# Performance work log

Measured on AMD Instinct MI355X. Metric: run time of the kernel, lower is better.

The kernel has to match this reference:

```python
import jax, jax.numpy as jnp
import numpy as np

V = 32000   # vocab_size
T = 2048    # train_len (pos embed table size)
E = 1024    # embed_dim
H = 16      # num_heads
FF = 4096   # ff_dim
L = 4       # num_layers
B, C = 2, 1024
D = E // H  # head_dim = 64
EPS = 1e-5


def setup_inputs() -> dict:
    key = jax.random.key(0)
    ks = jax.random.split(key, 12)
    s = 0.02
    inp = {
        "x": jax.random.randint(ks[0], (B, C), 0, V),
        "embed": jax.random.normal(ks[1], (V, E), jnp.float32) * s,
        "pos_embed": jax.random.normal(ks[2], (T, E), jnp.float32) * s,
        "Wq": jax.random.normal(ks[3], (L, E, E), jnp.float32) * s,
        "Wk": jax.random.normal(ks[4], (L, E, E), jnp.float32) * s,
        "Wv": jax.random.normal(ks[5], (L, E, E), jnp.float32) * s,
        "Wo": jax.random.normal(ks[6], (L, E, E), jnp.float32) * s,
        "ln1_w": jnp.ones((L, E), jnp.float32),
        "ln1_b": jnp.zeros((L, E), jnp.float32),
        "ln2_w": jnp.ones((L, E), jnp.float32),
        "ln2_b": jnp.zeros((L, E), jnp.float32),
        "W1": jax.random.normal(ks[7], (L, E, FF), jnp.float32) * s,
        "b1": jnp.zeros((L, FF), jnp.float32),
        "W2": jax.random.normal(ks[8], (L, FF, E), jnp.float32) * s,
        "b2": jnp.zeros((L, E), jnp.float32),
        "lnf_w": jnp.ones((E,), jnp.float32),
        "lnf_b": jnp.zeros((E,), jnp.float32),
        "Wout": jax.random.normal(ks[9], (E, V), jnp.float32) * s,
        "bout": jnp.zeros((V,), jnp.float32),
    }
    return inp


def _layernorm(h, w, b):
    mu = jnp.mean(h, axis=-1, keepdims=True)
    var = jnp.var(h, axis=-1, keepdims=True)
    return (h - mu) * jax.lax.rsqrt(var + EPS) * w + b


def reference(x, embed, pos_embed, Wq, Wk, Wv, Wo, ln1_w, ln1_b, ln2_w, ln2_b,
              W1, b1, W2, b2, lnf_w, lnf_b, Wout, bout):
    Bx, Cx = x.shape
    positions = jnp.clip(jnp.arange(Cx), 0, T - 1)  # 'clamp' extrapolation
    h = embed[x] + pos_embed[positions]             # [B,C,E]
    # causal mask: -inf above the diagonal
    mask = jnp.where(jnp.tril(jnp.ones((Cx, Cx), bool)), 0.0, -jnp.inf).astype(h.dtype)
    scale = 1.0 / np.sqrt(D)
    for i in range(L):
        hn = _layernorm(h, ln1_w[i], ln1_b[i])
        Q = (hn @ Wq[i]).reshape(Bx, Cx, H, D).transpose(0, 2, 1, 3)  # [B,H,C,D]
        K = (hn @ Wk[i]).reshape(Bx, Cx, H, D).transpose(0, 2, 1, 3)
        Vv = (hn @ Wv[i]).reshape(Bx, Cx, H, D).transpose(0, 2, 1, 3)
        scores = jnp.einsum('bhqd,bhkd->bhqk', Q, K) * scale + mask
        weights = jax.nn.softmax(scores, axis=-1)
        attn = jnp.einsum('bhqk,bhkd->bhqd', weights, Vv)
        attn = attn.transpose(0, 2, 1, 3).reshape(Bx, Cx, E) @ Wo[i]
        h = h + attn
        hn2 = _layernorm(h, ln2_w[i], ln2_b[i])
        h = h + jax.nn.gelu(hn2 @ W1[i] + b1[i], approximate=False) @ W2[i] + b2[i]
    return _layernorm(h, lnf_w, lnf_b) @ Wout + bout  # [B,C,V]
```

## Files before the change

kernel.cpp:

```cpp
#include <hip/hip_runtime.h>
#include <hip/hip_bf16.h>
#include <math.h>

constexpr int V  = 32000;
constexpr int E  = 1024;
constexpr int H  = 16;
constexpr int FF = 4096;
constexpr int L  = 4;
constexpr int B  = 2;
constexpr int C  = 1024;
constexpr int D  = 64;
constexpr int N  = B * C;
constexpr int E3 = 3 * E;
constexpr float EPS = 1e-5f;

typedef __hip_bfloat16 bf16;
typedef __bf16 bf16x8 __attribute__((ext_vector_type(8)));
typedef __bf16 bf16x4 __attribute__((ext_vector_type(4)));
typedef float  f32x4  __attribute__((ext_vector_type(4)));

#define AS1 __attribute__((address_space(1)))
#define AS3 __attribute__((address_space(3)))

__device__ inline bf16x8 lds_load8(const bf16* p) {
    bf16x4 lo = *(const bf16x4*)p;
    bf16x4 hi = *(const bf16x4*)(p + 4);
    bf16x8 r;
    r[0]=lo[0]; r[1]=lo[1]; r[2]=lo[2]; r[3]=lo[3];
    r[4]=hi[0]; r[5]=hi[1]; r[6]=hi[2]; r[7]=hi[3];
    return r;
}
__device__ inline void lds_store8(bf16* p, bf16x8 v) {
    bf16x4 lo, hi;
    lo[0]=v[0]; lo[1]=v[1]; lo[2]=v[2]; lo[3]=v[3];
    hi[0]=v[4]; hi[1]=v[5]; hi[2]=v[6]; hi[3]=v[7];
    *(bf16x4*)p = lo; *(bf16x4*)(p + 4) = hi;
}

__device__ inline bf16x8 lds_frag32(const bf16* sbase, int row, int c) {
    return *(const bf16x8*)(sbase + row * 32 + ((c ^ ((row >> 1) & 3)) << 3));
}
__device__ inline bf16x8 lds_frag64(const bf16* sbase, int row, int c) {
    return *(const bf16x8*)(sbase + row * 64 + ((c ^ (row & 7)) << 3));
}

__global__ void embed_kernel(const int* __restrict__ x,
                             const float* __restrict__ embed,
                             const float* __restrict__ pos,
                             float* __restrict__ h) {
    int token = blockIdx.x;
    int c = token % C;
    int id = x[token];
    const float* erow = embed + (size_t)id * E;
    const float* prow = pos   + (size_t)c  * E;
    float* hrow = h + (size_t)token * E;
    for (int e = threadIdx.x; e < E; e += blockDim.x)
        hrow[e] = erow[e] + prow[e];
}

__global__ void layernorm_kernel(const float* __restrict__ in,
                                 const float* __restrict__ w,
                                 const float* __restrict__ b,
                                 bf16* __restrict__ out) {
    __shared__ float red[256];
    int token = blockIdx.x;
    int tid = threadIdx.x;
    float4 xv = ((const float4*)(in + (size_t)token * E))[tid];

    red[tid] = xv.x + xv.y + xv.z + xv.w;
    __syncthreads();
    for (int st = 128; st > 0; st >>= 1) {
        if (tid < st) red[tid] += red[tid + st];
        __syncthreads();
    }
    float mu = red[0] * (1.0f / E);
    __syncthreads();

    float d0 = xv.x - mu, d1 = xv.y - mu, d2 = xv.z - mu, d3 = xv.w - mu;
    red[tid] = d0 * d0 + d1 * d1 + d2 * d2 + d3 * d3;
    __syncthreads();
    for (int st = 128; st > 0; st >>= 1) {
        if (tid < st) red[tid] += red[tid + st];
        __syncthreads();
    }
    float var = red[0] * (1.0f / E);
    float inv = rsqrtf(var + EPS);

    float4 wv = ((const float4*)w)[tid];
    float4 bv = ((const float4*)b)[tid];
    float y0 = d0 * inv * wv.x + bv.x;
    float y1 = d1 * inv * wv.y + bv.y;
    float y2 = d2 * inv * wv.z + bv.z;
    float y3 = d3 * inv * wv.w + bv.w;
    ushort4 o;
    { bf16 t0 = __float2bfloat16(y0); o.x = *(ushort*)&t0; }
    { bf16 t1 = __float2bfloat16(y1); o.y = *(ushort*)&t1; }
    { bf16 t2 = __float2bfloat16(y2); o.z = *(ushort*)&t2; }
    { bf16 t3 = __float2bfloat16(y3); o.w = *(ushort*)&t3; }
    ((ushort4*)(out + (size_t)token * E))[tid] = o;
}

__global__ void transpose_all(const float* __restrict__ Wq,
                              const float* __restrict__ Wk,
                              const float* __restrict__ Wv,
                              const float* __restrict__ Wo,
                              const float* __restrict__ W1,
                              const float* __restrict__ W2,
                              const float* __restrict__ Wout,
                              bf16* __restrict__ qkvt, bf16* __restrict__ wot,
                              bf16* __restrict__ w1t,  bf16* __restrict__ w2t,
                              bf16* __restrict__ wvt) {
    __shared__ float tile[64][65];
    int b = blockIdx.x;
    const float* src; bf16* dst;
    int Nn, Kk, n0, k0;
    if (b >= 12288) {
        int rem = b - 12288;
        src = Wout; dst = wvt; Nn = V; Kk = E;
        n0 = (rem % 500) * 64; k0 = (rem / 500) * 64;
    } else {
        int i = b / 3072, r = b % 3072;
        if (r < 1024) {
            int mat = r >> 8, rr = r & 255;
            n0 = (rr & 15) * 64; k0 = (rr >> 4) * 64;
            Nn = E; Kk = E;
            const float* srcs[4] = {Wq, Wk, Wv, Wo};
            src = srcs[mat] + (size_t)i * E * E;
            dst = (mat < 3) ? qkvt + ((size_t)i * E3 + (size_t)mat * E) * E
                            : wot + (size_t)i * E * E;
        } else if (r < 2048) {
            int rr = r - 1024;
            n0 = (rr & 63) * 64; k0 = (rr >> 6) * 64;
            Nn = FF; Kk = E;
            src = W1 + (size_t)i * E * FF;
            dst = w1t + (size_t)i * FF * E;
        } else {
            int rr = r - 2048;
            n0 = (rr & 15) * 64; k0 = (rr >> 4) * 64;
            Nn = E; Kk = FF;
            src = W2 + (size_t)i * FF * E;
            dst = w2t + (size_t)i * E * FF;
        }
    }
    int tid = threadIdx.x;
    #pragma unroll
    for (int it = 0; it < 4; ++it) {
        int idx = it * 256 + tid;
        int row = idx >> 4, c4 = (idx & 15) * 4;
        *(float4*)&tile[row][c4] =
            *(const float4*)&src[(size_t)(k0 + row) * Nn + n0 + c4];
    }
    __syncthreads();
    #pragma unroll
    for (int it = 0; it < 2; ++it) {
        int s = it * 256 + tid;
        int nrow = s >> 3, kc = s & 7;
        bf16x8 v;
        #pragma unroll
        for (int j = 0; j < 8; ++j)
            v[j] = (__bf16)__float2bfloat16(tile[kc * 8 + j][nrow]);
        *(bf16x8*)&dst[(size_t)(n0 + nrow) * Kk + k0 + kc * 8] = v;
    }
}

__global__ void transpose_v(const bf16* __restrict__ qkv,
                            bf16* __restrict__ vt) {
    __shared__ ushort tile[32][34];
    int c0 = blockIdx.x * 32;
    int d0 = (blockIdx.y & 1) * 32;
    int bh = blockIdx.y >> 1;
    int bb = bh >> 4, hh = bh & 15;
    int tx = threadIdx.x & 31, ty = threadIdx.x >> 5;
    const ushort* src = (const ushort*)qkv;
    ushort* dst = (ushort*)vt;
    #pragma unroll
    for (int i = 0; i < 32; i += 8)
        tile[ty + i][tx] = src[(size_t)(bb * C + c0 + ty + i) * E3 + 2 * E + hh * D + d0 + tx];
    __syncthreads();
    #pragma unroll
    for (int i = 0; i < 32; i += 8)
        dst[((size_t)bh * D + d0 + ty + i) * C + c0 + tx] = tile[tx][ty + i];
}

__launch_bounds__(512, 2)
__global__ void gemm_v8(const bf16* __restrict__ A,
                        const bf16* __restrict__ Bt,
                        const float* __restrict__ bias,
                        float* __restrict__ outF,
                        int M, int Nc, int K) {
    __shared__ __align__(16) bf16 sA[2][2][128 * 64];
    __shared__ __align__(16) bf16 sB[2][2][128 * 64];

    int tid  = threadIdx.x;
    int lane = tid & 63;
    int wid  = tid >> 6;
    int wm   = wid >> 2;
    int wn   = wid & 3;
    int l16  = lane & 15;
    int lhi  = lane >> 4;

    int nwg = gridDim.x * gridDim.y;
    int id  = blockIdx.y * gridDim.x + blockIdx.x;
    int cpx = nwg >> 3;
    int swz = (id & 7) * cpx + (id >> 3);
    int bx  = swz / gridDim.y;
    int by  = swz % gridDim.y;

    size_t brow = (size_t)by * 256;
    size_t bcol = (size_t)bx * 256;

    f32x4 acc[8][4] = {};

    auto stageA = [&](int buf, int half, int t) {
        size_t k0 = (size_t)t * 64;
        #pragma unroll
        for (int j = 0; j < 2; ++j) {
            int s = j * 512 + tid;
            int row = s >> 3;
            int ch  = (s & 7) ^ (row & 7);
            int ldso = (j * 512 + wid * 64) * 8;
            const bf16* g = A + (brow + half * 128 + row) * K + k0 + ch * 8;
            __builtin_amdgcn_global_load_lds(
                (const AS1 void*)g, (AS3 void*)(&sA[buf][half][0] + ldso), 16, 0, 0);
        }
    };
    auto stageB = [&](int buf, int half, int t) {
        size_t k0 = (size_t)t * 64;
        #pragma unroll
        for (int j = 0; j < 2; ++j) {
            int s = j * 512 + tid;
            int row = s >> 3;
            int ch  = (s & 7) ^ (row & 7);
            int ldso = (j * 512 + wid * 64) * 8;
            const bf16* g = Bt + (bcol + half * 128 + row) * K + k0 + ch * 8;
            __builtin_amdgcn_global_load_lds(
                (const AS1 void*)g, (AS3 void*)(&sB[buf][half][0] + ldso), 16, 0, 0);
        }
    };

    int NT = K / 64;
    stageA(0, 0, 0); stageB(0, 0, 0); stageB(0, 1, 0); stageA(0, 1, 0);

    bf16x8 ra[4][2], rb[2][2];

    for (int t = 0; t < NT; ++t) {
        int cur = t & 1, nxt = cur ^ 1;
        int ts = (t + 1 < NT) ? t + 1 : t;

        stageA(nxt, 0, ts);
        asm volatile("s_waitcnt vmcnt(6)" ::: "memory");
        __builtin_amdgcn_sched_barrier(0);
        __builtin_amdgcn_s_barrier();
        #pragma unroll
        for (int m = 0; m < 4; ++m)
            #pragma unroll
            for (int kh = 0; kh < 2; ++kh)
                ra[m][kh] = lds_frag64(&sA[cur][0][0], wm * 64 + m * 16 + l16, kh * 4 + lhi);
        #pragma unroll
        for (int n = 0; n < 2; ++n)
            #pragma unroll
            for (int kh = 0; kh < 2; ++kh)
                rb[n][kh] = lds_frag64(&sB[cur][0][0], wn * 32 + n * 16 + l16, kh * 4 + lhi);
        __builtin_amdgcn_s_setprio(1);
        #pragma unroll
        for (int m = 0; m < 4; ++m)
            #pragma unroll
            for (int n = 0; n < 2; ++n)
                #pragma unroll
                for (int kh = 0; kh < 2; ++kh)
                    acc[m][n] = __builtin_amdgcn_mfma_f32_16x16x32_bf16(
                        ra[m][kh], rb[n][kh], acc[m][n], 0, 0, 0);
        __builtin_amdgcn_s_setprio(0);

        stageB(nxt, 0, ts);
        asm volatile("s_waitcnt vmcnt(6)" ::: "memory");
        __builtin_amdgcn_sched_barrier(0);
        __builtin_amdgcn_s_barrier();
        #pragma unroll
        for (int n = 0; n < 2; ++n)
            #pragma unroll
            for (int kh = 0; kh < 2; ++kh)
                rb[n][kh] = lds_frag64(&sB[cur][1][0], wn * 32 + n * 16 + l16, kh * 4 + lhi);
        __builtin_amdgcn_s_setprio(1);
        #pragma unroll
        for (int m = 0; m < 4; ++m)
            #pragma unroll
            for (int n = 0; n < 2; ++n)
                #pragma unroll
                for (int kh = 0; kh < 2; ++kh)
                    acc[m][n + 2] = __builtin_amdgcn_mfma_f32_16x16x32_bf16(
                        ra[m][kh], rb[n][kh], acc[m][n + 2], 0, 0, 0);
        __builtin_amdgcn_s_setprio(0);

        stageB(nxt, 1, ts);
        asm volatile("s_waitcnt vmcnt(6)" ::: "memory");
        __builtin_amdgcn_sched_barrier(0);
        __builtin_amdgcn_s_barrier();
        #pragma unroll
        for (int m = 0; m < 4; ++m)
            #pragma unroll
            for (int kh = 0; kh < 2; ++kh)
                ra[m][kh] = lds_frag64(&sA[cur][1][0], wm * 64 + m * 16 + l16, kh * 4 + lhi);
        __builtin_amdgcn_s_setprio(1);
        #pragma unroll
        for (int m = 0; m < 4; ++m)
            #pragma unroll
            for (int n = 0; n < 2; ++n)
                #pragma unroll
                for (int kh = 0; kh < 2; ++kh)
                    acc[m + 4][n + 2] = __builtin_amdgcn_mfma_f32_16x16x32_bf16(
                        ra[m][kh], rb[n][kh], acc[m + 4][n + 2], 0, 0, 0);
        __builtin_amdgcn_s_setprio(0);

        stageA(nxt, 1, ts);
        asm volatile("s_waitcnt vmcnt(6)" ::: "memory");
        __builtin_amdgcn_sched_barrier(0);
        __builtin_amdgcn_s_barrier();
        #pragma unroll
        for (int n = 0; n < 2; ++n)
            #pragma unroll
            for (int kh = 0; kh < 2; ++kh)
                rb[n][kh] = lds_frag64(&sB[cur][0][0], wn * 32 + n * 16 + l16, kh * 4 + lhi);
        __builtin_amdgcn_s_setprio(1);
        #pragma unroll
        for (int m = 0; m < 4; ++m)
            #pragma unroll
            for (int n = 0; n < 2; ++n)
                #pragma unroll
                for (int kh = 0; kh < 2; ++kh)
                    acc[m + 4][n] = __builtin_amdgcn_mfma_f32_16x16x32_bf16(
                        ra[m][kh], rb[n][kh], acc[m + 4][n], 0, 0, 0);
        __builtin_amdgcn_s_setprio(0);
    }

    int crow = lhi * 4;
    #pragma unroll
    for (int qm = 0; qm < 2; ++qm)
        #pragma unroll
        for (int qn = 0; qn < 2; ++qn)
            #pragma unroll
            for (int m = 0; m < 4; ++m)
                #pragma unroll
                for (int n = 0; n < 2; ++n)
                    #pragma unroll
                    for (int r = 0; r < 4; ++r) {
                        size_t row = brow + qm * 128 + wm * 64 + m * 16 + crow + r;
                        size_t col = bcol + qn * 128 + wn * 32 + n * 16 + l16;
                        float val = acc[qm * 4 + m][qn * 2 + n][r];
                        val += bias[col];
                        outF[row * Nc + col] = val;
                    }
}

__launch_bounds__(256, 2)
__global__ void gemm_bf16_128(const bf16* __restrict__ A,
                              const bf16* __restrict__ Bt,
                              const float* __restrict__ bias,
                              const float* __restrict__ res,
                              float* __restrict__ outF,
                              bf16*  __restrict__ outB,
                              int M, int Nc, int K, int gelu_flag) {
    __shared__ __align__(16) bf16 sA[4][128 * 32];
    __shared__ __align__(16) bf16 sB[4][128 * 32];

    int tid  = threadIdx.x;
    int lane = tid & 63;
    int wid  = tid >> 6;
    int wr   = wid >> 1;
    int wc   = wid & 1;
    int l16  = lane & 15;
    int lhi  = lane >> 4;

    int nwg = gridDim.x * gridDim.y;
    int id  = blockIdx.y * gridDim.x + blockIdx.x;
    int cpx = nwg >> 3;
    int swz = (id & 7) * cpx + (id >> 3);
    int bx  = swz / gridDim.y;
    int by  = swz % gridDim.y;

    size_t brow = (size_t)by * 128;
    size_t bcol = (size_t)bx * 128;

    f32x4 acc[4][4] = {};

    auto stage = [&](int buf, int t) {
        size_t k0 = (size_t)t * 32;
        #pragma unroll
        for (int j = 0; j < 2; ++j) {
            int s = j * 256 + tid;
            int row = s >> 2;
            int ch  = (s & 3) ^ ((row >> 1) & 3);
            int ldso = (j * 256 + wid * 64) * 8;
            const bf16* ga = A + (brow + row) * K + k0 + ch * 8;
            __builtin_amdgcn_global_load_lds(
                (const AS1 void*)ga, (AS3 void*)(&sA[buf][0] + ldso), 16, 0, 0);
        }
        #pragma unroll
        for (int j = 0; j < 2; ++j) {
            int s = j * 256 + tid;
            int row = s >> 2;
            int ch  = (s & 3) ^ ((row >> 1) & 3);
            int ldso = (j * 256 + wid * 64) * 8;
            const bf16* gb = Bt + (bcol + row) * K + k0 + ch * 8;
            __builtin_amdgcn_global_load_lds(
                (const AS1 void*)gb, (AS3 void*)(&sB[buf][0] + ldso), 16, 0, 0);
        }
    };

    int NT = K / 32;
    stage(0, 0);
    stage(1, 1);

    for (int t = 0; t < NT; ++t) {
        if (t + 2 < NT) {
            stage((t + 2) & 3, t + 2);
            asm volatile("s_waitcnt vmcnt(8)" ::: "memory");
        } else if (t + 1 < NT) {
            asm volatile("s_waitcnt vmcnt(4)" ::: "memory");
        } else {
            asm volatile("s_waitcnt vmcnt(0)" ::: "memory");
        }
        __builtin_amdgcn_sched_barrier(0);
        __builtin_amdgcn_s_barrier();

        const bf16* As_ = &sA[t & 3][0];
        const bf16* Bs_ = &sB[t & 3][0];
        bf16x8 ra[4], rb[4];
        #pragma unroll
        for (int m = 0; m < 4; ++m)
            ra[m] = lds_frag32(As_, wr * 64 + m * 16 + l16, lhi);
        #pragma unroll
        for (int n = 0; n < 4; ++n)
            rb[n] = lds_frag32(Bs_, wc * 64 + n * 16 + l16, lhi);

        __builtin_amdgcn_s_setprio(1);
        #pragma unroll
        for (int m = 0; m < 4; ++m)
            #pragma unroll
            for (int n = 0; n < 4; ++n)
                acc[m][n] = __builtin_amdgcn_mfma_f32_16x16x32_bf16(
                    ra[m], rb[n], acc[m][n], 0, 0, 0);
        __builtin_amdgcn_s_setprio(0);
    }

    int crow = lhi * 4;
    #pragma unroll
    for (int m = 0; m < 4; ++m) {
        #pragma unroll
        for (int n = 0; n < 4; ++n) {
            #pragma unroll
            for (int r = 0; r < 4; ++r) {
                size_t row = brow + wr * 64 + m * 16 + crow + r;
                size_t col = bcol + wc * 64 + n * 16 + l16;
                float val = acc[m][n][r];
                if (bias) val += bias[col];
                if (gelu_flag) val = 0.5f * val * (1.0f + erff(val * 0.70710678118f));
                if (res) val += res[row * Nc + col];
                if (outF) outF[row * Nc + col] = val;
                if (outB) outB[row * Nc + col] = __float2bfloat16(val);
            }
        }
    }
}

__launch_bounds__(256, 3)
__global__ void gemm_bf16_64(const bf16* __restrict__ A,
                             const bf16* __restrict__ Bt,
                             const float* __restrict__ bias,
                             const float* __restrict__ res,
                             float* __restrict__ outF,
                             bf16*  __restrict__ outB,
                             int M, int Nc, int K, int gelu_flag) {
    __shared__ __align__(16) bf16 sA[4][64 * 32];
    __shared__ __align__(16) bf16 sB[4][128 * 32];

    int tid  = threadIdx.x;
    int lane = tid & 63;
    int wid  = tid >> 6;
    int l16  = lane & 15;
    int lhi  = lane >> 4;

    int nwg = gridDim.x * gridDim.y;
    int id  = blockIdx.y * gridDim.x + blockIdx.x;
    int cpx = nwg >> 3;
    int swz = (id & 7) * cpx + (id >> 3);
    int bx  = swz / gridDim.y;
    int by  = swz % gridDim.y;

    size_t brow = (size_t)by * 64;
    size_t bcol = (size_t)bx * 128;

    f32x4 acc[4][2] = {};

    auto stage = [&](int buf, int t) {
        size_t k0 = (size_t)t * 32;
        {
            int s = tid;
            int row = s >> 2;
            int ch  = (s & 3) ^ ((row >> 1) & 3);
            int ldso = (wid * 64) * 8;
            const bf16* ga = A + (brow + row) * K + k0 + ch * 8;
            __builtin_amdgcn_global_load_lds(
                (const AS1 void*)ga, (AS3 void*)(&sA[buf][0] + ldso), 16, 0, 0);
        }
        #pragma unroll
        for (int j = 0; j < 2; ++j) {
            int s = j * 256 + tid;
            int row = s >> 2;
            int ch  = (s & 3) ^ ((row >> 1) & 3);
            int ldso = (j * 256 + wid * 64) * 8;
            const bf16* gb = Bt + (bcol + row) * K + k0 + ch * 8;
            __builtin_amdgcn_global_load_lds(
                (const AS1 void*)gb, (AS3 void*)(&sB[buf][0] + ldso), 16, 0, 0);
        }
    };

    int NT = K / 32;
    stage(0, 0);
    stage(1, 1);

    for (int t = 0; t < NT; ++t) {
        if (t + 2 < NT) {
            stage((t + 2) & 3, t + 2);
            asm volatile("s_waitcnt vmcnt(6)" ::: "memory");
        } else if (t + 1 < NT) {
            asm volatile("s_waitcnt vmcnt(3)" ::: "memory");
        } else {
            asm volatile("s_waitcnt vmcnt(0)" ::: "memory");
        }
        __builtin_amdgcn_sched_barrier(0);
        __builtin_amdgcn_s_barrier();

        const bf16* As_ = &sA[t & 3][0];
        const bf16* Bs_ = &sB[t & 3][0];
        bf16x8 ra[4], rb[2];
        #pragma unroll
        for (int m = 0; m < 4; ++m)
            ra[m] = lds_frag32(As_, m * 16 + l16, lhi);
        #pragma unroll
        for (int n = 0; n < 2; ++n)
            rb[n] = lds_frag32(Bs_, wid * 32 + n * 16 + l16, lhi);

        __builtin_amdgcn_s_setprio(1);
        #pragma unroll
        for (int m = 0; m < 4; ++m)
            #pragma unroll
            for (int n = 0; n < 2; ++n)
                acc[m][n] = __builtin_amdgcn_mfma_f32_16x16x32_bf16(
                    ra[m], rb[n], acc[m][n], 0, 0, 0);
        __builtin_amdgcn_s_setprio(0);
    }

    int crow = lhi * 4;
    #pragma unroll
    for (int m = 0; m < 4; ++m) {
        #pragma unroll
        for (int n = 0; n < 2; ++n) {
            #pragma unroll
            for (int r = 0; r < 4; ++r) {
                size_t row = brow + m * 16 + crow + r;
                size_t col = bcol + wid * 32 + n * 16 + l16;
                float val = acc[m][n][r];
                if (bias) val += bias[col];
                if (gelu_flag) val = 0.5f * val * (1.0f + erff(val * 0.70710678118f));
                if (res) val += res[row * Nc + col];
                if (outF) outF[row * Nc + col] = val;
                if (outB) outB[row * Nc + col] = __float2bfloat16(val);
            }
        }
    }
}

constexpr int QBLK = 128;
constexpr int KVB  = 64;
constexpr int PSTR = 72;

__launch_bounds__(512)
__global__ void flash_attn(const bf16* __restrict__ qkv,
                           const bf16* __restrict__ vt,
                           bf16* __restrict__ O) {
    __shared__ bf16 sK[KVB][PSTR];
    __shared__ bf16 sV[D][PSTR];
    __shared__ bf16 sP[8][16][PSTR];

    int qt = blockIdx.x;
    int bh = blockIdx.y;
    int bb = bh >> 4, hh = bh & 15;
    int qbase = qt * QBLK;
    int tid = threadIdx.x, lane = tid & 63, w = tid >> 6;
    int l16 = lane & 15, lhi = lane >> 4;

    int qrow = qbase + w * 16 + l16;
    const bf16* qp = qkv + (size_t)(bb * C + qrow) * E3 + hh * D + lhi * 8;
    bf16x8 qf0 = *(const bf16x8*)qp;
    bf16x8 qf1 = *(const bf16x8*)(qp + 32);

    f32x4 oa[4] = {};
    float m_run[4] = {-INFINITY, -INFINITY, -INFINITY, -INFINITY};
    float l_run[4] = {0.f, 0.f, 0.f, 0.f};

    int NTk = 2 * qt + 2;
    for (int t = 0; t < NTk; ++t) {
        int k0 = t * KVB;
        {
            int row = tid >> 3, c8 = tid & 7;
            bf16x8 kv = *(const bf16x8*)(qkv + (size_t)(bb * C + k0 + row) * E3 + E + hh * D + c8 * 8);
            lds_store8(&sK[row][c8 * 8], kv);
            bf16x8 vv = *(const bf16x8*)(vt + ((size_t)bh * D + row) * C + k0 + c8 * 8);
            lds_store8(&sV[row][c8 * 8], vv);
        }
        __syncthreads();

        f32x4 sc[4] = {};
        #pragma unroll
        for (int n = 0; n < 4; ++n) {
            bf16x8 kf0 = lds_load8(&sK[n * 16 + l16][lhi * 8]);
            sc[n] = __builtin_amdgcn_mfma_f32_16x16x32_bf16(qf0, kf0, sc[n], 0, 0, 0);
            bf16x8 kf1 = lds_load8(&sK[n * 16 + l16][32 + lhi * 8]);
            sc[n] = __builtin_amdgcn_mfma_f32_16x16x32_bf16(qf1, kf1, sc[n], 0, 0, 0);
        }

        int qg = qbase + w * 16 + lhi * 4;
        #pragma unroll
        for (int n = 0; n < 4; ++n) {
            int kg = k0 + n * 16 + l16;
            #pragma unroll
            for (int r = 0; r < 4; ++r) {
                float vvv = sc[n][r] * 0.125f;
                if (t >= 2 * qt && kg > qg + r) vvv = -1e30f;
                sc[n][r] = vvv;
            }
        }

        float pm[4];
        #pragma unroll
        for (int r = 0; r < 4; ++r)
            pm[r] = fmaxf(fmaxf(sc[0][r], sc[1][r]), fmaxf(sc[2][r], sc[3][r]));
        #pragma unroll
        for (int xm = 1; xm <= 8; xm <<= 1)
            #pragma unroll
            for (int r = 0; r < 4; ++r)
                pm[r] = fmaxf(pm[r], __shfl_xor(pm[r], xm));

        float corr[4];
        #pragma unroll
        for (int r = 0; r < 4; ++r) {
            float mn = fmaxf(m_run[r], pm[r]);
            corr[r] = __expf(m_run[r] - mn);
            m_run[r] = mn;
        }
        f32x4 p[4];
        #pragma unroll
        for (int n = 0; n < 4; ++n)
            #pragma unroll
            for (int r = 0; r < 4; ++r)
                p[n][r] = __expf(sc[n][r] - m_run[r]);

        float rsum[4];
        #pragma unroll
        for (int r = 0; r < 4; ++r)
            rsum[r] = p[0][r] + p[1][r] + p[2][r] + p[3][r];
        #pragma unroll
        for (int xm = 1; xm <= 8; xm <<= 1)
            #pragma unroll
            for (int r = 0; r < 4; ++r)
                rsum[r] += __shfl_xor(rsum[r], xm);
        #pragma unroll
        for (int r = 0; r < 4; ++r)
            l_run[r] = l_run[r] * corr[r] + rsum[r];
        #pragma unroll
        for (int nd = 0; nd < 4; ++nd)
            #pragma unroll
            for (int r = 0; r < 4; ++r)
                oa[nd][r] *= corr[r];

        #pragma unroll
        for (int n = 0; n < 4; ++n)
            #pragma unroll
            for (int r = 0; r < 4; ++r)
                sP[w][lhi * 4 + r][n * 16 + l16] = __float2bfloat16(p[n][r]);
        bf16x8 pa0 = lds_load8(&sP[w][l16][lhi * 8]);
        bf16x8 pa1 = lds_load8(&sP[w][l16][32 + lhi * 8]);

        #pragma unroll
        for (int nd = 0; nd < 4; ++nd) {
            bf16x8 vf0 = lds_load8(&sV[nd * 16 + l16][lhi * 8]);
            oa[nd] = __builtin_amdgcn_mfma_f32_16x16x32_bf16(pa0, vf0, oa[nd], 0, 0, 0);
            bf16x8 vf1 = lds_load8(&sV[nd * 16 + l16][32 + lhi * 8]);
            oa[nd] = __builtin_amdgcn_mfma_f32_16x16x32_bf16(pa1, vf1, oa[nd], 0, 0, 0);
        }
        __syncthreads();
    }

    #pragma unroll
    for (int r = 0; r < 4; ++r) {
        float inv = 1.0f / l_run[r];
        int qg = qbase + w * 16 + lhi * 4 + r;
        bf16* orow = O + (size_t)(bb * C + qg) * E + hh * D;
        #pragma unroll
        for (int nd = 0; nd < 4; ++nd)
            orow[nd * 16 + l16] = __float2bfloat16(oa[nd][r] * inv);
    }
}

extern "C" void kernel_launch(void* const* d_in, const int* in_sizes, int n_in,
                              void* d_out, int out_size, void* d_ws, size_t ws_size,
                              hipStream_t stream) {
    const int*   x     = (const int*)  d_in[0];
    const float* embed = (const float*)d_in[1];
    const float* pos   = (const float*)d_in[2];
    const float* Wq    = (const float*)d_in[3];
    const float* Wk    = (const float*)d_in[4];
    const float* Wv    = (const float*)d_in[5];
    const float* Wo    = (const float*)d_in[6];
    const float* ln1w  = (const float*)d_in[7];
    const float* ln1b  = (const float*)d_in[8];
    const float* ln2w  = (const float*)d_in[9];
    const float* ln2b  = (const float*)d_in[10];
    const float* W1    = (const float*)d_in[11];
    const float* b1    = (const float*)d_in[12];
    const float* W2    = (const float*)d_in[13];
    const float* b2    = (const float*)d_in[14];
    const float* lnfw  = (const float*)d_in[15];
    const float* lnfb  = (const float*)d_in[16];
    const float* Wout  = (const float*)d_in[17];
    const float* bout  = (const float*)d_in[18];
    float* out = (float*)d_out;

    char* p = (char*)d_ws;
    auto alloc = [&](size_t bytes) {
        char* r = p;
        p += (bytes + 255) & ~(size_t)255;
        return r;
    };
    float* h    = (float*)alloc((size_t)N * E  * 4);
    bf16*  qkvb = (bf16*) alloc((size_t)N * E3 * 2);
    bf16*  hn   = (bf16*) alloc((size_t)N * E  * 2);
    bf16*  attn = (bf16*) alloc((size_t)N * E  * 2);
    bf16*  ff   = (bf16*) alloc((size_t)N * FF * 2);
    bf16*  vt   = (bf16*) alloc((size_t)B * H * D * C * 2);
    bf16*  qkvt = (bf16*) alloc((size_t)L * E3 * E * 2);
    bf16*  wot  = (bf16*) alloc((size_t)L * E  * E * 2);
    bf16*  w1t  = (bf16*) alloc((size_t)L * FF * E * 2);
    bf16*  w2t  = (bf16*) alloc((size_t)L * E  * FF * 2);
    bf16*  wvt  = (bf16*) alloc((size_t)V * E  * 2 + 4096);

    transpose_all<<<20288, 256, 0, stream>>>(Wq, Wk, Wv, Wo, W1, W2, Wout,
                                             qkvt, wot, w1t, w2t, wvt);

    embed_kernel<<<N, 256, 0, stream>>>(x, embed, pos, h);

    dim3 gQKV(E3 / 128, N / 128);
    dim3 gF  (FF / 128, N / 128);
    dim3 gV  (V  / 256, N / 256);
    dim3 gO  (E  / 128, N / 64);

    for (int i = 0; i < L; ++i) {
        layernorm_kernel<<<N, 256, 0, stream>>>(h, ln1w + i * E, ln1b + i * E, hn);

        gemm_bf16_128<<<gQKV, 256, 0, stream>>>(hn, qkvt + (size_t)i * E3 * E,
                                                nullptr, nullptr, nullptr, qkvb,
                                                N, E3, E, 0);

        transpose_v<<<dim3(C / 32, 2 * B * H), 256, 0, stream>>>(qkvb, vt);

        flash_attn<<<dim3(C / QBLK, B * H), 512, 0, stream>>>(qkvb, vt, attn);

        gemm_bf16_64<<<gO, 256, 0, stream>>>(attn, wot + (size_t)i * E * E,
                                             nullptr, h, h, nullptr,
                                             N, E, E, 0);

        layernorm_kernel<<<N, 256, 0, stream>>>(h, ln2w + i * E, ln2b + i * E, hn);

        gemm_bf16_128<<<gF, 256, 0, stream>>>(hn, w1t + (size_t)i * FF * E,
                                              b1 + (size_t)i * FF, nullptr,
                                              nullptr, ff,
                                              N, FF, E, 1);
        gemm_bf16_64<<<gO, 256, 0, stream>>>(ff, w2t + (size_t)i * E * FF,
                                             b2 + (size_t)i * E, h, h, nullptr,
                                             N, E, FF, 0);
    }

    layernorm_kernel<<<N, 256, 0, stream>>>(h, lnfw, lnfb, hn);
    gemm_v8<<<gV, 512, 0, stream>>>(hn, wvt, bout, out, N, V, E);
}
```

Baseline: 1.244 ms.

## Restructure GEMM main loop to prefetch deeper and use two barriers per K-step

Reworks the 256x256 GEMM K-loop so half-tiles for step t+1 and t+2 are issued earlier, waits at vmcnt(8) instead of vmcnt(6), and cuts barriers from four to two per iteration. The B half-0 fragment is kept in a separate register set (rb0) so it no longer has to be reloaded from LDS for the last quadrant. The aim is to hide global-to-LDS latency and reduce synchronisation stalls. In exchange it uses more VGPRs and needs careful buffer reuse: stage t+2 is written into the current buffer while later quadrants may still read it, which risks a race.

```diff
diff --git a/kernel.cpp b/kernel.cpp
--- a/kernel.cpp
+++ b/kernel.cpp
@@ -239,18 +239,20 @@
     };
 
     int NT = K / 64;
-    stageA(0, 0, 0); stageB(0, 0, 0); stageB(0, 1, 0); stageA(0, 1, 0);
-
-    bf16x8 ra[4][2], rb[2][2];
+    stageA(0, 0, 0); stageB(0, 0, 0);
+    stageB(0, 1, 0); stageA(0, 1, 0);
+    stageA(1, 0, 1); stageB(1, 0, 1);
+
+    bf16x8 ra[4][2], rb[2][2], rb0[2][2];
 
     for (int t = 0; t < NT; ++t) {
         int cur = t & 1, nxt = cur ^ 1;
-        int ts = (t + 1 < NT) ? t + 1 : t;
-
-        stageA(nxt, 0, ts);
-        asm volatile("s_waitcnt vmcnt(6)" ::: "memory");
+
+        if (t == NT - 1) asm volatile("s_waitcnt vmcnt(4)" ::: "memory");
+        else             asm volatile("s_waitcnt vmcnt(8)" ::: "memory");
         __builtin_amdgcn_sched_barrier(0);
         __builtin_amdgcn_s_barrier();
+        if (t + 1 < NT) { stageB(nxt, 1, t + 1); stageA(nxt, 1, t + 1); }
         #pragma unroll
         for (int m = 0; m < 4; ++m)
             #pragma unroll
@@ -260,7 +262,7 @@
         for (int n = 0; n < 2; ++n)
             #pragma unroll
             for (int kh = 0; kh < 2; ++kh)
-                rb[n][kh] = lds_frag64(&sB[cur][0][0], wn * 32 + n * 16 + l16, kh * 4 + lhi);
+                rb0[n][kh] = lds_frag64(&sB[cur][0][0], wn * 32 + n * 16 + l16, kh * 4 + lhi);
         __builtin_amdgcn_s_setprio(1);
         #pragma unroll
         for (int m = 0; m < 4; ++m)
@@ -269,11 +271,11 @@
                 #pragma unroll
                 for (int kh = 0; kh < 2; ++kh)
                     acc[m][n] = __builtin_amdgcn_mfma_f32_16x16x32_bf16(
-                        ra[m][kh], rb[n][kh], acc[m][n], 0, 0, 0);
+                        ra[m][kh], rb0[n][kh], acc[m][n], 0, 0, 0);
         __builtin_amdgcn_s_setprio(0);
 
-        stageB(nxt, 0, ts);
-        asm volatile("s_waitcnt vmcnt(6)" ::: "memory");
+        if (t == NT - 1) asm volatile("s_waitcnt vmcnt(0)" ::: "memory");
+        else             asm volatile("s_waitcnt vmcnt(8)" ::: "memory");
         __builtin_amdgcn_sched_barrier(0);
         __builtin_amdgcn_s_barrier();
         #pragma unroll
@@ -292,10 +294,7 @@
                         ra[m][kh], rb[n][kh], acc[m][n + 2], 0, 0, 0);
         __builtin_amdgcn_s_setprio(0);
 
-        stageB(nxt, 1, ts);
-        asm volatile("s_waitcnt vmcnt(6)" ::: "memory");
-        __builtin_amdgcn_sched_barrier(0);
-        __builtin_amdgcn_s_barrier();
+        if (t + 2 < NT) { stageA(cur, 0, t + 2); stageB(cur, 0, t + 2); }
         #pragma unroll
         for (int m = 0; m < 4; ++m)
             #pragma unroll
@@ -312,15 +311,6 @@
                         ra[m][kh], rb[n][kh], acc[m + 4][n + 2], 0, 0, 0);
         __builtin_amdgcn_s_setprio(0);
 
-        stageA(nxt, 1, ts);
-        asm volatile("s_waitcnt vmcnt(6)" ::: "memory");
-        __builtin_amdgcn_sched_barrier(0);
-        __builtin_amdgcn_s_barrier();
-        #pragma unroll
-        for (int n = 0; n < 2; ++n)
-            #pragma unroll
-            for (int kh = 0; kh < 2; ++kh)
-                rb[n][kh] = lds_frag64(&sB[cur][0][0], wn * 32 + n * 16 + l16, kh * 4 + lhi);
         __builtin_amdgcn_s_setprio(1);
         #pragma unroll
         for (int m = 0; m < 4; ++m)
@@ -329,7 +319,7 @@
                 #pragma unroll
                 for (int kh = 0; kh < 2; ++kh)
                     acc[m + 4][n] = __builtin_amdgcn_mfma_f32_16x16x32_bf16(
-                        ra[m][kh], rb[n][kh], acc[m + 4][n], 0, 0, 0);
+                        ra[m][kh], rb0[n][kh], acc[m + 4][n], 0, 0, 0);
         __builtin_amdgcn_s_setprio(0);
     }
 
```

New measurement: 1.239 ms. About the same (-0.4%).
